# Performance work log

Hardware: AMD Instinct MI355X
Metric: run time of the kernel (lower is better)

## Reference

```python
import jax, jax.numpy as jnp
import numpy as np

EPS = 1e-08
F_DIM = 512


def setup_inputs() -> dict:
    key = jax.random.key(0)
    ks = jax.random.split(key, 7)
    N, F = 50000, F_DIM
    q = jax.random.normal(ks[0], (N, 1, F), dtype=jnp.float32)
    mu = jax.random.normal(ks[1], (N, 3, F), dtype=jnp.float32)
    # Xavier-ish scaled params
    W_mix = jax.random.normal(ks[2], (2 * F, F), dtype=jnp.float32) * (1.0 / np.sqrt(F))
    W1 = jax.random.normal(ks[3], (F, 2 * F), dtype=jnp.float32) * (1.0 / np.sqrt(2 * F))
    b1 = jnp.zeros((F,), dtype=jnp.float32)
    W2 = jax.random.normal(ks[4], (3 * F, F), dtype=jnp.float32) * (1.0 / np.sqrt(F))
    b2 = jnp.zeros((3 * F,), dtype=jnp.float32)
    return {"q": q, "mu": mu, "W_mix": W_mix, "W1": W1, "b1": b1, "W2": W2, "b2": b2}


def reference(q, mu, W_mix, W1, b1, W2, b2):
    F = q.shape[-1]
    # mu_channel_mix: [N,3,F] @ [F,2F] -> [N,3,2F]
    mu_mix = jnp.einsum('ndf,gf->ndg', mu, W_mix)
    mu_V, mu_W = mu_mix[..., :F], mu_mix[..., F:]
    # vector norm over Cartesian axis -> [N,1,F]
    mu_Vn = jnp.sqrt(jnp.sum(mu_V * mu_V, axis=-2, keepdims=True) + EPS)
    ctx = jnp.concatenate([q, mu_Vn], axis=-1)  # [N,1,2F]
    h = jax.nn.silu(jnp.einsum('nsf,gf->nsg', ctx, W1) + b1)  # [N,1,F]
    x = jnp.einsum('nsf,gf->nsg', h, W2) + b2  # [N,1,3F]
    dq_intra = x[..., :F]
    dmu_intra = x[..., F:2 * F] * mu_W  # broadcast [N,1,F]*[N,3,F]
    dqmu_intra = x[..., 2 * F:] * jnp.sum(mu_V * mu_W, axis=1, keepdims=True)
    q_out = q + dq_intra + dqmu_intra
    mu_out = mu + dmu_intra
    return (q_out, mu_out)
```

## Files before the change

### kernel.cpp

```cpp
#include <hip/hip_runtime.h>
#include <stdint.h>

#define NN 50000
#define QWORDS 25600000

typedef __attribute__((ext_vector_type(8))) short bf16x8;
typedef __attribute__((ext_vector_type(4))) float f32x4;

__device__ __forceinline__ uint32_t f2bf(float x){
  uint32_t u = __builtin_bit_cast(uint32_t, x);
  u += 0x7FFFu + ((u >> 16) & 1u);
  return u >> 16;
}
__device__ __forceinline__ float bf2f(uint32_t b){
  uint32_t u = b << 16;
  return __builtin_bit_cast(float, u);
}
__device__ __forceinline__ void gload16(const uint16_t* g, uint16_t* l){
  __builtin_amdgcn_global_load_lds(
      (const __attribute__((address_space(1))) uint32_t*)g,
      (__attribute__((address_space(3))) uint32_t*)l, 16, 0, 0);
}
__device__ __forceinline__ f32x4 mfma16(bf16x8 a, bf16x8 b, f32x4 c){
  return __builtin_amdgcn_mfma_f32_16x16x32_bf16(a, b, c, 0, 0, 0);
}

#define FENCE() asm volatile("" ::: "memory")

__global__ void k_convert(const float* __restrict__ wmix, const float* __restrict__ w1,
                          const float* __restrict__ w2, uint16_t* __restrict__ dst){
  int i = blockIdx.x * 256 + threadIdx.x;
  int e = i << 2;
  const float* s; int o;
  if (e < 524288)       { s = wmix; o = e; }
  else if (e < 1048576) { s = w1;   o = e - 524288; }
  else                  { s = w2;   o = e - 1048576; }
  f32x4 v = *(const f32x4*)(s + o);
  uint2 pk;
  pk.x = f2bf(v[0]) | (f2bf(v[1]) << 16);
  pk.y = f2bf(v[2]) | (f2bf(v[3]) << 16);
  *(uint2*)(dst + e) = pk;
}

__global__ __launch_bounds__(256, 2)
void k_gemm1(const float* __restrict__ mu, const uint16_t* __restrict__ wmixb,
             uint16_t* __restrict__ qh, float* __restrict__ muW){
  __shared__ uint16_t As[2][12288];
  __shared__ uint16_t Bs[2][8192];
  const int tid  = threadIdx.x;
  const int lane = tid & 63;
  const int w    = tid >> 6;
  const int orig = blockIdx.x;
  const int j    = (orig & 7) * 782 + (orig >> 3);
  const int f0   = (j & 7) * 64;
  const int n0   = (j >> 3) * 64;
  const int si = tid >> 4;
  const int sc = (tid & 15) * 4;

  f32x4 ar[12];
  auto A_LOAD = [&](int ks){
    const int k0 = ks * 64;
    #pragma unroll
    for (int blk=0; blk<4; ++blk)
      #pragma unroll
      for (int d=0; d<3; ++d){
        int n = n0 + blk*16 + si;
        int g = (n < NN ? n : NN-1)*3 + d;
        ar[blk*3+d] = *(const f32x4*)(mu + (size_t)g*512 + k0 + sc);
      }
  };
  auto A_WRITE = [&](int buf){
    #pragma unroll
    for (int blk=0; blk<4; ++blk)
      #pragma unroll
      for (int d=0; d<3; ++d){
        int r = blk*48 + d*16 + si;
        f32x4 v = ar[blk*3+d];
        uint2 pk;
        pk.x = f2bf(v[0]) | (f2bf(v[1]) << 16);
        pk.y = f2bf(v[2]) | (f2bf(v[3]) << 16);
        *(uint2*)&As[buf][r*64 + (sc ^ ((r&7)<<3))] = pk;
      }
  };
  auto B_ISSUE = [&](int ks, int buf){
    const int k0 = ks * 64;
    #pragma unroll
    for (int jj=0; jj<4; ++jj){
      int jb = w*4 + jj;
      int row = jb*8 + (lane>>3);
      int g = (row < 64) ? (f0 + row) : (448 + f0 + row);
      int srcc = ((lane&7) ^ ((lane>>3)&7)) * 8;
      gload16(wmixb + (size_t)g*512 + k0 + srcc, &Bs[buf][jb*512]);
    }
  };

  const f32x4 z4 = {0.f,0.f,0.f,0.f};
  f32x4 acc[3][8];
  #pragma unroll
  for (int d=0; d<3; ++d)
    #pragma unroll
    for (int nt=0; nt<8; ++nt) acc[d][nt] = z4;

  A_LOAD(0); B_ISSUE(0, 0); A_WRITE(0);
  for (int ks=0; ks<8; ++ks){
    const int cur = ks & 1;
    __syncthreads();
    if (ks < 7){ A_LOAD(ks+1); B_ISSUE(ks+1, cur^1); }
    #pragma unroll
    for (int kf=0; kf<2; ++kf){
      int kc = kf*32 + (lane>>4)*8;
      bf16x8 af[3];
      #pragma unroll
      for (int d=0; d<3; ++d){
        int r = w*48 + d*16 + (lane&15);
        af[d] = *(const bf16x8*)&As[cur][r*64 + (kc ^ ((r&7)<<3))];
      }
      #pragma unroll
      for (int nt=0; nt<8; ++nt){
        int rr = nt*16 + (lane&15);
        bf16x8 bf = *(const bf16x8*)&Bs[cur][rr*64 + (kc ^ ((rr&7)<<3))];
        #pragma unroll
        for (int d=0; d<3; ++d)
          acc[d][nt] = mfma16(af[d], bf, acc[d][nt]);
      }
    }
    if (ks < 7) A_WRITE(cur^1);
  }

  const int rb4 = (lane >> 4) * 4;
  #pragma unroll
  for (int c=0; c<4; ++c){
    #pragma unroll
    for (int jx=0; jx<4; ++jx){
      int n = n0 + w*16 + rb4 + jx;
      if (n >= NN) continue;
      int f = f0 + c*16 + (lane & 15);
      float v0 = acc[0][c][jx],   v1 = acc[1][c][jx],   v2 = acc[2][c][jx];
      float u0 = acc[0][c+4][jx], u1 = acc[1][c+4][jx], u2 = acc[2][c+4][jx];
      float vn = sqrtf(v0*v0 + v1*v1 + v2*v2 + 1e-8f);
      float dt = v0*u0 + v1*u1 + v2*u2;
      qh[(size_t)n*1024 + f]       = (uint16_t)f2bf(vn);
      qh[(size_t)n*1024 + 512 + f] = (uint16_t)f2bf(dt);
      size_t mb = (size_t)n*1536 + f;
      muW[mb] = u0; muW[mb+512] = u1; muW[mb+1024] = u2;
    }
  }
}

__global__ __launch_bounds__(256, 2)
void k_gemm2(const float* __restrict__ q, const uint16_t* __restrict__ w1b,
             const float* __restrict__ b1, uint16_t* __restrict__ qh){
  __shared__ uint16_t A2[2][2048];
  __shared__ uint16_t B2[2][16384];
  const int tid  = threadIdx.x;
  const int lane = tid & 63;
  const int w    = tid >> 6;
  const int wm   = w >> 1;
  const int wn   = w & 1;
  const int n0   = blockIdx.x * 64;

  f32x4 qa0, qa1;
  auto QA_LOAD = [&](int s){
    int k0 = s*32;
    int row = tid >> 2, ch = tid & 3;
    int nc = (n0 + row < NN) ? n0 + row : NN-1;
    qa0 = *(const f32x4*)(q + (size_t)nc*512 + k0 + ch*8);
    qa1 = *(const f32x4*)(q + (size_t)nc*512 + k0 + ch*8 + 4);
  };
  auto QA_WRITE = [&](int buf){
    int row = tid >> 2, ch = tid & 3;
    uint4 pk;
    pk.x = f2bf(qa0[0]) | (f2bf(qa0[1]) << 16);
    pk.y = f2bf(qa0[2]) | (f2bf(qa0[3]) << 16);
    pk.z = f2bf(qa1[0]) | (f2bf(qa1[1]) << 16);
    pk.w = f2bf(qa1[2]) | (f2bf(qa1[3]) << 16);
    *(uint4*)&A2[buf][row*32 + ((ch ^ (row&3)))*8] = pk;
  };
  auto VA_ISSUE = [&](int s, int buf){
    int k0v = (s-16)*32;
    int row = w*16 + (lane>>2);
    int nc = (n0 + row < NN) ? n0 + row : NN-1;
    int srcch = (lane&3) ^ (row&3);
    gload16(qh + (size_t)nc*1024 + k0v + srcch*8, &A2[buf][w*512]);
  };
  auto B_ISSUE = [&](int s, int buf){
    int k0 = s*32;
    #pragma unroll
    for (int jj=0; jj<8; ++jj){
      int j = w*8 + jj;
      int row = j*16 + (lane>>2);
      int srcch = (lane&3) ^ (row&3);
      gload16(w1b + (size_t)row*1024 + k0 + srcch*8, &B2[buf][j*512]);
    }
  };

  const f32x4 z4 = {0.f,0.f,0.f,0.f};
  f32x4 acc2[2][16];
  #pragma unroll
  for (int mt=0; mt<2; ++mt)
    #pragma unroll
    for (int nt=0; nt<16; ++nt) acc2[mt][nt] = z4;

  QA_LOAD(0); B_ISSUE(0, 0); QA_WRITE(0);
  for (int s=0; s<32; ++s){
    const int cur = s & 1;
    __syncthreads();
    if (s < 31){
      if (s+1 < 16) QA_LOAD(s+1); else VA_ISSUE(s+1, cur^1);
      B_ISSUE(s+1, cur^1);
    }
    {
      int kc = (lane>>4)*8;
      bf16x8 a[2];
      #pragma unroll
      for (int mt=0; mt<2; ++mt){
        int r = wm*32 + mt*16 + (lane&15);
        a[mt] = *(const bf16x8*)&A2[cur][r*32 + (kc ^ ((r&3)<<3))];
      }
      #pragma unroll
      for (int nt=0; nt<16; ++nt){
        int rr = wn*256 + nt*16 + (lane&15);
        bf16x8 b = *(const bf16x8*)&B2[cur][rr*32 + (kc ^ ((rr&3)<<3))];
        acc2[0][nt] = mfma16(a[0], b, acc2[0][nt]);
        acc2[1][nt] = mfma16(a[1], b, acc2[1][nt]);
      }
    }
    if (s < 31 && s+1 < 16) QA_WRITE(cur^1);
  }

  const int rb4 = (lane >> 4) * 4;
  #pragma unroll
  for (int nt=0; nt<16; ++nt){
    int col = wn*256 + nt*16 + (lane&15);
    float bb = b1[col];
    #pragma unroll
    for (int mt=0; mt<2; ++mt)
      #pragma unroll
      for (int j=0; j<4; ++j){
        int n = n0 + wm*32 + mt*16 + rb4 + j;
        if (n < NN){
          float x = acc2[mt][nt][j] + bb;
          float sv = x / (1.f + __expf(-x));
          qh[(size_t)n*1024 + col] = (uint16_t)f2bf(sv);
        }
      }
  }
}

__global__ __launch_bounds__(512, 1)
void k_gemm3(const float* __restrict__ q, const float* __restrict__ mu,
             const uint16_t* __restrict__ w2b, const float* __restrict__ b2,
             float* __restrict__ dout){
  __shared__ uint16_t Hs[64*512];
  __shared__ uint16_t B3[3][12288];
  const int tid  = threadIdx.x;
  const int lane = tid & 63;
  const int w    = tid >> 6;
  const int wm   = w >> 2;
  const int wn   = w & 3;
  const int n0   = blockIdx.x * 64;
  const uint16_t* qh = (const uint16_t*)dout;
  float* mout = dout + (size_t)QWORDS;
  const int l15 = lane & 15;
  const int rb4 = (lane >> 4) * 4;
  const f32x4 z4 = {0.f,0.f,0.f,0.f};

  #pragma unroll
  for (int i=0; i<8; ++i){
    int row = w*8 + i;
    int nc = (n0 + row < NN) ? n0 + row : NN-1;
    gload16(qh + (size_t)nc*1024 + (size_t)((lane ^ (row&7))*8), &Hs[row*512]);
  }

  auto B_ISSUE = [&](int it, int ks, uint16_t* slot){
    #pragma unroll
    for (int jj=0; jj<3; ++jj){
      int j = w*3 + jj;
      int rr = j*8 + (lane>>3);
      int s3 = rr >> 6, fi = rr & 63;
      int g = s3*512 + it*64 + fi;
      gload16(w2b + (size_t)g*512 + ks*64 + ((lane&7) ^ (rr&7))*8, slot + j*512);
    }
  };
  B_ISSUE(0, 0, B3[0]);
  B_ISSUE(0, 1, B3[1]);

  float dtv[8], qv[8], muv[3][8], mwv[3][8];
  float bb0=0.f, bb1=0.f, bb2=0.f;
  int   fq = 0;
  f32x4 acc3[2][3];
  int rs = 0;

#define K3_PREF(KS) do{ \
    int t2 = it*8 + (KS) + 2; \
    int itc = (t2 < 64) ? (t2 >> 3) : 0; \
    int ksc = t2 & 7; \
    int is = rs + 2; if (is >= 3) is -= 3; \
    B_ISSUE(itc, ksc, B3[is]); \
  } while(0)

#define K3_MFMA(KS) do{ \
    const uint16_t* bsl = B3[rs]; \
    __builtin_amdgcn_s_setprio(1); \
    _Pragma("unroll") \
    for (int kf=0; kf<2; ++kf){ \
      bf16x8 a[2]; \
      _Pragma("unroll") \
      for (int mt=0; mt<2; ++mt){ \
        int r = wm*32 + mt*16 + l15; \
        int ch = ((KS)*8 + kf*4 + (lane>>4)) ^ (r&7); \
        a[mt] = *(const bf16x8*)&Hs[r*512 + ch*8]; \
      } \
      _Pragma("unroll") \
      for (int s3=0; s3<3; ++s3){ \
        int rr = s3*64 + wn*16 + l15; \
        int ch = (kf*4 + (lane>>4)) ^ (rr&7); \
        bf16x8 b = *(const bf16x8*)&bsl[rr*64 + ch*8]; \
        acc3[0][s3] = mfma16(a[0], b, acc3[0][s3]); \
        acc3[1][s3] = mfma16(a[1], b, acc3[1][s3]); \
      } \
    } \
    __builtin_amdgcn_s_setprio(0); \
  } while(0)

#define K3_ADV() do{ rs = (rs + 1 < 3) ? rs + 1 : 0; } while(0)

  #pragma unroll 1
  for (int it=0; it<8; ++it){
    if (it) { asm volatile("s_waitcnt vmcnt(35)" ::: "memory"); }
    else    { asm volatile("s_waitcnt vmcnt(3)"  ::: "memory"); }
    __builtin_amdgcn_s_barrier();
    K3_PREF(0);
    FENCE();
    {
      #pragma unroll
      for (int mt=0; mt<2; ++mt)
        #pragma unroll
        for (int s3=0; s3<3; ++s3) acc3[mt][s3] = z4;
      fq = it*64 + wn*16 + l15;
      bb0 = b2[fq]; bb1 = b2[512+fq]; bb2 = b2[1024+fq];
      #pragma unroll
      for (int p=0; p<8; ++p){
        int n = n0 + wm*32 + (p>>2)*16 + rb4 + (p&3);
        int nc = n < NN ? n : NN-1;
        dtv[p] = bf2f(qh[(size_t)nc*1024 + 512 + fq]);
        qv[p]  = q[(size_t)nc*512 + fq];
      }
    }
    FENCE();
    K3_MFMA(0); K3_ADV();

    if (it) { asm volatile("s_waitcnt vmcnt(54)" ::: "memory"); }
    else    { asm volatile("s_waitcnt vmcnt(22)" ::: "memory"); }
    __builtin_amdgcn_s_barrier();
    K3_PREF(1);
    FENCE();
    {
      #pragma unroll
      for (int p=0; p<8; ++p){
        int n = n0 + wm*32 + (p>>2)*16 + rb4 + (p&3);
        int nc = n < NN ? n : NN-1;
        size_t mb = (size_t)nc*1536 + fq;
        muv[0][p] = mu[mb]; muv[1][p] = mu[mb+512]; muv[2][p] = mu[mb+1024];
      }
    }
    FENCE();
    K3_MFMA(1); K3_ADV();

    asm volatile("s_waitcnt vmcnt(46)" ::: "memory");
    __builtin_amdgcn_s_barrier();
    K3_PREF(2);
    FENCE();
    {
      #pragma unroll
      for (int p=0; p<8; ++p){
        int n = n0 + wm*32 + (p>>2)*16 + rb4 + (p&3);
        int nc = n < NN ? n : NN-1;
        size_t mb = (size_t)nc*1536 + fq;
        mwv[0][p] = mout[mb]; mwv[1][p] = mout[mb+512]; mwv[2][p] = mout[mb+1024];
      }
    }
    FENCE();
    K3_MFMA(2); K3_ADV();

    asm volatile("s_waitcnt vmcnt(51)" ::: "memory");
    __builtin_amdgcn_s_barrier();
    K3_PREF(3);
    FENCE();
    K3_MFMA(3); K3_ADV();

    asm volatile("s_waitcnt vmcnt(27)" ::: "memory");
    __builtin_amdgcn_s_barrier();
    K3_PREF(4);
    FENCE();
    K3_MFMA(4); K3_ADV();

    asm volatile("s_waitcnt vmcnt(3)" ::: "memory");
    __builtin_amdgcn_s_barrier();
    K3_PREF(5);
    FENCE();
    K3_MFMA(5); K3_ADV();

    asm volatile("s_waitcnt vmcnt(3)" ::: "memory");
    __builtin_amdgcn_s_barrier();
    K3_PREF(6);
    FENCE();
    K3_MFMA(6); K3_ADV();

    asm volatile("s_waitcnt vmcnt(3)" ::: "memory");
    __builtin_amdgcn_s_barrier();
    K3_PREF(7);
    FENCE();
    K3_MFMA(7);
    {
      #pragma unroll
      for (int p=0; p<8; ++p){
        int n = n0 + wm*32 + (p>>2)*16 + rb4 + (p&3);
        if (n < NN){
          float x0 = acc3[p>>2][0][p&3] + bb0;
          float x1 = acc3[p>>2][1][p&3] + bb1;
          float x2 = acc3[p>>2][2][p&3] + bb2;
          dout[(size_t)n*512 + fq] = qv[p] + x0 + x2*dtv[p];
          size_t mb = (size_t)n*1536 + fq;
          mout[mb]      = muv[0][p] + x1*mwv[0][p];
          mout[mb+512]  = muv[1][p] + x1*mwv[1][p];
          mout[mb+1024] = muv[2][p] + x1*mwv[2][p];
        }
      }
    }
    K3_ADV();
  }
#undef K3_PREF
#undef K3_MFMA
#undef K3_ADV
}

extern "C" void kernel_launch(void* const* d_in, const int* in_sizes, int n_in,
                              void* d_out, int out_size, void* d_ws, size_t ws_size,
                              hipStream_t stream){
  (void)in_sizes; (void)n_in; (void)out_size; (void)ws_size;
  const float* q    = (const float*)d_in[0];
  const float* mu   = (const float*)d_in[1];
  const float* wmix = (const float*)d_in[2];
  const float* w1   = (const float*)d_in[3];
  const float* b1   = (const float*)d_in[4];
  const float* w2   = (const float*)d_in[5];
  const float* b2   = (const float*)d_in[6];
  uint16_t* wb = (uint16_t*)d_ws;
  float* dout = (float*)d_out;

  hipLaunchKernelGGL(k_convert, dim3(1792), dim3(256), 0, stream, wmix, w1, w2, wb);
  hipLaunchKernelGGL(k_gemm1, dim3(6256), dim3(256), 0, stream,
                     mu, wb, (uint16_t*)d_out, dout + (size_t)QWORDS);
  hipLaunchKernelGGL(k_gemm2, dim3(782), dim3(256), 0, stream,
                     q, wb + 524288, b1, (uint16_t*)d_out);
  hipLaunchKernelGGL(k_gemm3, dim3(782), dim3(512), 0, stream,
                     q, mu, wb + 1048576, b2, dout);
}
```

Measured before the change: 989.8 us.

## Halve gemm3 row tile and switch to double-buffered B for higher occupancy

Shrinks the final GEMM's per-block row tile from 64 to 32 and doubles the grid. LDS drops from a triple-buffered to a double-buffered weight ring, and launch bounds are raised so more blocks can co-reside per CU. This is meant to improve latency hiding and load balance through occupancy. In exchange, each weight tile is reused by half as many rows, L2 weight traffic doubles, and the shallower prefetch adds full vmcnt(0) waits.

```diff
diff --git a/kernel.cpp b/kernel.cpp
--- a/kernel.cpp
+++ b/kernel.cpp
@@ -247,18 +247,18 @@
   }
 }
 
-__global__ __launch_bounds__(512, 1)
+__global__ __launch_bounds__(512, 4)
 void k_gemm3(const float* __restrict__ q, const float* __restrict__ mu,
              const uint16_t* __restrict__ w2b, const float* __restrict__ b2,
              float* __restrict__ dout){
-  __shared__ uint16_t Hs[64*512];
-  __shared__ uint16_t B3[3][12288];
+  __shared__ uint16_t Hs[32*512];
+  __shared__ uint16_t B3[2][12288];
   const int tid  = threadIdx.x;
   const int lane = tid & 63;
   const int w    = tid >> 6;
   const int wm   = w >> 2;
   const int wn   = w & 3;
-  const int n0   = blockIdx.x * 64;
+  const int n0   = blockIdx.x * 32;
   const uint16_t* qh = (const uint16_t*)dout;
   float* mout = dout + (size_t)QWORDS;
   const int l15 = lane & 15;
@@ -266,8 +266,8 @@
   const f32x4 z4 = {0.f,0.f,0.f,0.f};
 
   #pragma unroll
-  for (int i=0; i<8; ++i){
-    int row = w*8 + i;
+  for (int i=0; i<4; ++i){
+    int row = w*4 + i;
     int nc = (n0 + row < NN) ? n0 + row : NN-1;
     gload16(qh + (size_t)nc*1024 + (size_t)((lane ^ (row&7))*8), &Hs[row*512]);
   }
@@ -283,143 +283,123 @@
     }
   };
   B_ISSUE(0, 0, B3[0]);
-  B_ISSUE(0, 1, B3[1]);
-
-  float dtv[8], qv[8], muv[3][8], mwv[3][8];
+
+  float dtv[4], qv[4], muv[3][4], mwv[3][4];
   float bb0=0.f, bb1=0.f, bb2=0.f;
   int   fq = 0;
-  f32x4 acc3[2][3];
-  int rs = 0;
-
-#define K3_PREF(KS) do{ \
-    int t2 = it*8 + (KS) + 2; \
-    int itc = (t2 < 64) ? (t2 >> 3) : 0; \
-    int ksc = t2 & 7; \
-    int is = rs + 2; if (is >= 3) is -= 3; \
-    B_ISSUE(itc, ksc, B3[is]); \
-  } while(0)
+  f32x4 acc3[3];
 
 #define K3_MFMA(KS) do{ \
-    const uint16_t* bsl = B3[rs]; \
+    const uint16_t* bsl = B3[(KS)&1]; \
     __builtin_amdgcn_s_setprio(1); \
     _Pragma("unroll") \
     for (int kf=0; kf<2; ++kf){ \
-      bf16x8 a[2]; \
-      _Pragma("unroll") \
-      for (int mt=0; mt<2; ++mt){ \
-        int r = wm*32 + mt*16 + l15; \
-        int ch = ((KS)*8 + kf*4 + (lane>>4)) ^ (r&7); \
-        a[mt] = *(const bf16x8*)&Hs[r*512 + ch*8]; \
-      } \
+      int r = wm*16 + l15; \
+      int ch = ((KS)*8 + kf*4 + (lane>>4)) ^ (r&7); \
+      bf16x8 a = *(const bf16x8*)&Hs[r*512 + ch*8]; \
       _Pragma("unroll") \
       for (int s3=0; s3<3; ++s3){ \
         int rr = s3*64 + wn*16 + l15; \
-        int ch = (kf*4 + (lane>>4)) ^ (rr&7); \
-        bf16x8 b = *(const bf16x8*)&bsl[rr*64 + ch*8]; \
-        acc3[0][s3] = mfma16(a[0], b, acc3[0][s3]); \
-        acc3[1][s3] = mfma16(a[1], b, acc3[1][s3]); \
+        int chb = (kf*4 + (lane>>4)) ^ (rr&7); \
+        bf16x8 b = *(const bf16x8*)&bsl[rr*64 + chb*8]; \
+        acc3[s3] = mfma16(a, b, acc3[s3]); \
       } \
     } \
     __builtin_amdgcn_s_setprio(0); \
   } while(0)
 
-#define K3_ADV() do{ rs = (rs + 1 < 3) ? rs + 1 : 0; } while(0)
-
   #pragma unroll 1
   for (int it=0; it<8; ++it){
-    if (it) { asm volatile("s_waitcnt vmcnt(35)" ::: "memory"); }
-    else    { asm volatile("s_waitcnt vmcnt(3)"  ::: "memory"); }
-    __builtin_amdgcn_s_barrier();
-    K3_PREF(0);
+    if (it) { asm volatile("s_waitcnt vmcnt(16)" ::: "memory"); }
+    else    { asm volatile("s_waitcnt vmcnt(0)"  ::: "memory"); }
+    __builtin_amdgcn_s_barrier();
+    B_ISSUE(it, 1, B3[1]);
     FENCE();
     {
       #pragma unroll
-      for (int mt=0; mt<2; ++mt)
-        #pragma unroll
-        for (int s3=0; s3<3; ++s3) acc3[mt][s3] = z4;
+      for (int s3=0; s3<3; ++s3) acc3[s3] = z4;
       fq = it*64 + wn*16 + l15;
       bb0 = b2[fq]; bb1 = b2[512+fq]; bb2 = b2[1024+fq];
       #pragma unroll
-      for (int p=0; p<8; ++p){
-        int n = n0 + wm*32 + (p>>2)*16 + rb4 + (p&3);
+      for (int p=0; p<4; ++p){
+        int n = n0 + wm*16 + rb4 + p;
         int nc = n < NN ? n : NN-1;
         dtv[p] = bf2f(qh[(size_t)nc*1024 + 512 + fq]);
         qv[p]  = q[(size_t)nc*512 + fq];
       }
     }
     FENCE();
-    K3_MFMA(0); K3_ADV();
-
-    if (it) { asm volatile("s_waitcnt vmcnt(54)" ::: "memory"); }
-    else    { asm volatile("s_waitcnt vmcnt(22)" ::: "memory"); }
-    __builtin_amdgcn_s_barrier();
-    K3_PREF(1);
+    K3_MFMA(0);
+
+    asm volatile("s_waitcnt vmcnt(11)" ::: "memory");
+    __builtin_amdgcn_s_barrier();
+    B_ISSUE(it, 2, B3[0]);
     FENCE();
     {
       #pragma unroll
-      for (int p=0; p<8; ++p){
-        int n = n0 + wm*32 + (p>>2)*16 + rb4 + (p&3);
+      for (int p=0; p<4; ++p){
+        int n = n0 + wm*16 + rb4 + p;
         int nc = n < NN ? n : NN-1;
         size_t mb = (size_t)nc*1536 + fq;
         muv[0][p] = mu[mb]; muv[1][p] = mu[mb+512]; muv[2][p] = mu[mb+1024];
       }
     }
     FENCE();
-    K3_MFMA(1); K3_ADV();
-
-    asm volatile("s_waitcnt vmcnt(46)" ::: "memory");
-    __builtin_amdgcn_s_barrier();
-    K3_PREF(2);
+    K3_MFMA(1);
+
+    asm volatile("s_waitcnt vmcnt(12)" ::: "memory");
+    __builtin_amdgcn_s_barrier();
+    B_ISSUE(it, 3, B3[1]);
     FENCE();
     {
       #pragma unroll
-      for (int p=0; p<8; ++p){
-        int n = n0 + wm*32 + (p>>2)*16 + rb4 + (p&3);
+      for (int p=0; p<4; ++p){
+        int n = n0 + wm*16 + rb4 + p;
         int nc = n < NN ? n : NN-1;
         size_t mb = (size_t)nc*1536 + fq;
         mwv[0][p] = mout[mb]; mwv[1][p] = mout[mb+512]; mwv[2][p] = mout[mb+1024];
       }
     }
     FENCE();
-    K3_MFMA(2); K3_ADV();
-
-    asm volatile("s_waitcnt vmcnt(51)" ::: "memory");
-    __builtin_amdgcn_s_barrier();
-    K3_PREF(3);
-    FENCE();
-    K3_MFMA(3); K3_ADV();
-
-    asm volatile("s_waitcnt vmcnt(27)" ::: "memory");
-    __builtin_amdgcn_s_barrier();
-    K3_PREF(4);
-    FENCE();
-    K3_MFMA(4); K3_ADV();
-
-    asm volatile("s_waitcnt vmcnt(3)" ::: "memory");
-    __builtin_amdgcn_s_barrier();
-    K3_PREF(5);
-    FENCE();
-    K3_MFMA(5); K3_ADV();
-
-    asm volatile("s_waitcnt vmcnt(3)" ::: "memory");
-    __builtin_amdgcn_s_barrier();
-    K3_PREF(6);
-    FENCE();
-    K3_MFMA(6); K3_ADV();
-
-    asm volatile("s_waitcnt vmcnt(3)" ::: "memory");
-    __builtin_amdgcn_s_barrier();
-    K3_PREF(7);
+    K3_MFMA(2);
+
+    asm volatile("s_waitcnt vmcnt(12)" ::: "memory");
+    __builtin_amdgcn_s_barrier();
+    B_ISSUE(it, 4, B3[0]);
+    FENCE();
+    K3_MFMA(3);
+
+    asm volatile("s_waitcnt vmcnt(0)" ::: "memory");
+    __builtin_amdgcn_s_barrier();
+    B_ISSUE(it, 5, B3[1]);
+    FENCE();
+    K3_MFMA(4);
+
+    asm volatile("s_waitcnt vmcnt(0)" ::: "memory");
+    __builtin_amdgcn_s_barrier();
+    B_ISSUE(it, 6, B3[0]);
+    FENCE();
+    K3_MFMA(5);
+
+    asm volatile("s_waitcnt vmcnt(0)" ::: "memory");
+    __builtin_amdgcn_s_barrier();
+    B_ISSUE(it, 7, B3[1]);
+    FENCE();
+    K3_MFMA(6);
+
+    asm volatile("s_waitcnt vmcnt(0)" ::: "memory");
+    __builtin_amdgcn_s_barrier();
+    if (it < 7) B_ISSUE(it+1, 0, B3[0]);
     FENCE();
     K3_MFMA(7);
     {
       #pragma unroll
-      for (int p=0; p<8; ++p){
-        int n = n0 + wm*32 + (p>>2)*16 + rb4 + (p&3);
+      for (int p=0; p<4; ++p){
+        int n = n0 + wm*16 + rb4 + p;
         if (n < NN){
-          float x0 = acc3[p>>2][0][p&3] + bb0;
-          float x1 = acc3[p>>2][1][p&3] + bb1;
-          float x2 = acc3[p>>2][2][p&3] + bb2;
+          float x0 = acc3[0][p] + bb0;
+          float x1 = acc3[1][p] + bb1;
+          float x2 = acc3[2][p] + bb2;
           dout[(size_t)n*512 + fq] = qv[p] + x0 + x2*dtv[p];
           size_t mb = (size_t)n*1536 + fq;
           mout[mb]      = muv[0][p] + x1*mwv[0][p];
@@ -428,11 +408,8 @@
         }
       }
     }
-    K3_ADV();
-  }
-#undef K3_PREF
+  }
 #undef K3_MFMA
-#undef K3_ADV
 }
 
 extern "C" void kernel_launch(void* const* d_in, const int* in_sizes, int n_in,
@@ -454,6 +431,6 @@
                      mu, wb, (uint16_t*)d_out, dout + (size_t)QWORDS);
   hipLaunchKernelGGL(k_gemm2, dim3(782), dim3(256), 0, stream,
                      q, wb + 524288, b1, (uint16_t*)d_out);
-  hipLaunchKernelGGL(k_gemm3, dim3(782), dim3(512), 0, stream,
+  hipLaunchKernelGGL(k_gemm3, dim3(1563), dim3(512), 0, stream,
                      q, mu, wb + 1048576, b2, dout);
 }
```

After: 929.8 us. -6.1%, faster.
